# Optimization experiments

Measured on AMD Instinct MI355X. Metric: run time of the kernel, lower is better.

## Reference

```python
import jax, jax.numpy as jnp
import numpy as np

# Dimensions inferred from the module (few-shot reweighted YOLOv2 region loss)
B, C, NA, NCPA = 64, 20, 5, 1          # batch, base classes, anchors, classes-per-anchor
H, W = 19, 19                           # feature map (608 input / stride 32)
T = 50                                  # cfg.max_boxes
THRESH = 0.6
COORD_SCALE = 1.0
CLASS_SCALE = 1.0
NB = B * C                              # per-class 'image' rows, as in the torch code
A4 = NA * H * W
EPS = 1e-12
BCE_EPS = 1e-7
ANCHORS = [[1.3221, 1.73145], [3.19275, 4.00944], [5.05587, 8.09892], [9.47112, 4.84053], [11.2364, 10.0071]]


def iou_xywh(x1, y1, w1, h1, x2, y2, w2, h2):
    # center-size IoU, matches darknet bbox_iou(x1y1x2y2=False)
    l = jnp.maximum(x1 - w1 * 0.5, x2 - w2 * 0.5)
    r = jnp.minimum(x1 + w1 * 0.5, x2 + w2 * 0.5)
    t = jnp.maximum(y1 - h1 * 0.5, y2 - h2 * 0.5)
    b = jnp.minimum(y1 + h1 * 0.5, y2 + h2 * 0.5)
    inter = jnp.clip(r - l, 0.0) * jnp.clip(b - t, 0.0)
    union = w1 * h1 + w2 * h2 - inter
    return inter / jnp.maximum(union, EPS)


def setup_inputs() -> dict:
    key = jax.random.key(0)
    k1, k2, k3, k4 = jax.random.split(key, 4)
    output = jax.random.normal(k1, (NB, NA * (5 + NCPA), H, W), jnp.float32) * 0.5
    # target rows: [cls, x, y, w, h] * T, coords in (0,1); x kept > 0 so all boxes are 'valid'
    cls_ids = jax.random.randint(k2, (B, C, T), 0, C).astype(jnp.float32)
    xy = jax.random.uniform(k3, (B, C, T, 2), minval=0.05, maxval=0.95)
    wh = jax.random.uniform(k4, (B, C, T, 2), minval=0.05, maxval=0.5)
    target = jnp.concatenate([cls_ids[..., None], xy, wh], axis=-1).reshape(B, C, T * 5)
    anchors = jnp.asarray(ANCHORS, jnp.float32)
    return {"output": output, "target": target, "anchors": anchors}


def _forward(output, target, anchors):
    target = jax.lax.stop_gradient(target)
    anchors = jax.lax.stop_gradient(anchors)
    out5 = output.reshape(NB, NA, 5 + NCPA, H, W)
    x = jax.nn.sigmoid(out5[:, :, 0])
    y = jax.nn.sigmoid(out5[:, :, 1])
    w = out5[:, :, 2]
    h = out5[:, :, 3]
    conf = jax.nn.sigmoid(out5[:, :, 4])
    # class logits regrouped to original batch: (B*NA*H*W, C)
    cls = out5[:, :, 5:5 + NCPA].reshape(NB, NA, H, W)
    cls_logits = cls.reshape(B, C, NA * H * W).transpose(0, 2, 1).reshape(-1, C)
    # decode pred boxes (detached, mirroring torch's use of .data)
    grid_x = jnp.arange(W, dtype=jnp.float32)[None, None, None, :]
    grid_y = jnp.arange(H, dtype=jnp.float32)[None, None, :, None]
    aw = anchors[:, 0][None, :, None, None]
    ah = anchors[:, 1][None, :, None, None]
    px = jax.lax.stop_gradient(x) + grid_x
    py = jax.lax.stop_gradient(y) + grid_y
    pw = jnp.exp(jax.lax.stop_gradient(w)) * aw
    ph = jnp.exp(jax.lax.stop_gradient(h)) * ah
    # ground-truth boxes per row
    tgt = target.reshape(NB, T, 5)
    cls_t = tgt[:, :, 0]
    gx = tgt[:, :, 1] * W
    gy = tgt[:, :, 2] * H
    gw = tgt[:, :, 3] * W
    gh = tgt[:, :, 4] * H
    # 'break on first zero x' semantics
    valid = jnp.cumprod((tgt[:, :, 1] != 0).astype(jnp.int32), axis=1) > 0
    # stage 1: zero conf_mask where any gt IoU > thresh (scan over T to avoid (NB,T,A4) blowup)
    pxf = px.reshape(NB, A4); pyf = py.reshape(NB, A4)
    pwf = pw.reshape(NB, A4); phf = ph.reshape(NB, A4)

    def iou_step(ci, xs):
        gxt, gyt, gwt, ght, vt = xs
        iou = iou_xywh(pxf, pyf, pwf, phf, gxt[:, None], gyt[:, None], gwt[:, None], ght[:, None])
        return jnp.maximum(ci, jnp.where(vt[:, None], iou, 0.0)), None

    cur_ious, _ = jax.lax.scan(iou_step, jnp.zeros((NB, A4), jnp.float32), (gx.T, gy.T, gw.T, gh.T, valid.T))
    conf_mask0 = jnp.where(cur_ious.reshape(NB, NA, H, W) > THRESH, 0.0, 1.0)
    # best anchor per gt by wh-only IoU
    inter = jnp.minimum(gw[..., None], anchors[:, 0]) * jnp.minimum(gh[..., None], anchors[:, 1])
    union = gw[..., None] * gh[..., None] + anchors[:, 0] * anchors[:, 1] - inter
    best_n = jnp.argmax(inter / jnp.maximum(union, EPS), axis=-1).astype(jnp.int32)  # (NB,T)
    gi = gx.astype(jnp.int32)
    gj = gy.astype(jnp.int32)
    # stage 2: ordered scatter of targets (later boxes overwrite earlier, as in the torch loops)
    binds = jnp.arange(NB)
    z = jnp.zeros((NB, NA, H, W), jnp.float32)
    # seen < 12800 branch: tx=ty=0.5, tw=th=0, coord_mask=1
    carry0 = (jnp.ones_like(z), z, conf_mask0, jnp.full_like(z, 0.5), jnp.full_like(z, 0.5), z, z, z, z)

    def tgt_step(carry, xs):
        cm, clm, cfm, tx, ty, tw, th, tconf, tcls = carry
        gxt, gyt, gwt, ght, bn, git, gjt, vt, ct = xs
        idx = (binds, bn, gjt, git)

        def upd(arr, val):
            return arr.at[idx].set(jnp.where(vt, val, arr[idx]))

        aw_b = anchors[bn, 0]
        ah_b = anchors[bn, 1]
        iou = iou_xywh(gxt, gyt, gwt, ght, px[idx], py[idx], pw[idx], ph[idx])
        cm = upd(cm, 1.0)
        clm = upd(clm, 1.0)
        cfm = upd(cfm, 1.0)
        tx = upd(tx, gxt - git.astype(jnp.float32))
        ty = upd(ty, gyt - gjt.astype(jnp.float32))
        tw = upd(tw, jnp.log(jnp.maximum(gwt, EPS) / aw_b))
        th = upd(th, jnp.log(jnp.maximum(ght, EPS) / ah_b))
        tconf = upd(tconf, iou)
        tcls = upd(tcls, ct)
        return (cm, clm, cfm, tx, ty, tw, th, tconf, tcls), None

    xs = (gx.T, gy.T, gw.T, gh.T, best_n.T, gi.T, gj.T, valid.T, cls_t.T)
    (coord_mask, cls_mask, conf_mask, tx, ty, tw, th, tconf, tcls), _ = jax.lax.scan(tgt_step, carry0, xs)
    # regroup per-class rows back to original batch (neg_ratio='full' -> counts[i] == C)
    cm_grp = cls_mask.reshape(B, C, NA, H, W).sum(axis=1)
    tcls_grp = tcls.reshape(B, C, NA, H, W).sum(axis=1)
    sel = (cm_grp == 1.0).reshape(-1)           # exclude colliding cells
    labels = tcls_grp.reshape(-1).astype(jnp.int32)

    def bce_mean(p, t):
        p = jnp.clip(p, BCE_EPS, 1.0 - BCE_EPS)
        return jnp.mean(-(t * jnp.log(p) + (1.0 - t) * jnp.log(1.0 - p)))

    loss_x = COORD_SCALE * bce_mean(x * coord_mask, tx * coord_mask)
    loss_y = COORD_SCALE * bce_mean(y * coord_mask, ty * coord_mask)
    loss_w = COORD_SCALE * 0.5 * jnp.mean((w * coord_mask - tw * coord_mask) ** 2)
    loss_h = COORD_SCALE * 0.5 * jnp.mean((h * coord_mask - th * coord_mask) ** 2)
    loss_conf = 0.5 * jnp.mean((conf * conf_mask - tconf * conf_mask) ** 2)
    logp = jax.nn.log_softmax(cls_logits, axis=-1)
    nll = -jnp.take_along_axis(logp, labels[:, None], axis=1)[:, 0]
    nsel = jnp.maximum(jnp.sum(sel.astype(jnp.float32)), 1.0)
    loss_cls = CLASS_SCALE * jnp.sum(jnp.where(sel, nll, 0.0)) / nsel
    return loss_x + loss_y + loss_w + loss_h + loss_conf + loss_cls


def reference(output, target, anchors):
    return _forward(output, target, anchors)
```

## Files before the change

kernel.cpp:

```cpp
#include <hip/hip_runtime.h>
#include <math.h>

constexpr int cB   = 64;
constexpr int cC   = 20;
constexpr int cNA  = 5;
constexpr int cH   = 19;
constexpr int cW   = 19;
constexpr int cT   = 50;
constexpr int cNB  = cB * cC;
constexpr int cHW  = cH * cW;
constexpr int cA4  = cNA * cHW;
constexpr int cCH  = cNA * 6;
constexpr long cNTOT = (long)cNB * cA4;
constexpr int cCLS_ROWS = cB * cA4;

constexpr int ACC_BANKS = 64;
constexpr int TGT_N   = cNB * cT;
constexpr size_t SZT   = (size_t)TGT_N * 4;
constexpr size_t OFF_GX  = 4096;
constexpr size_t OFF_GY  = OFF_GX  + SZT;
constexpr size_t OFF_GW  = OFF_GY  + SZT;
constexpr size_t OFF_GH  = OFF_GW  + SZT;
constexpr size_t OFF_CLS = OFF_GH  + SZT;
constexpr size_t OFF_BL  = OFF_CLS + SZT;
constexpr size_t OFF_BR  = OFF_BL  + SZT;
constexpr size_t OFF_BT  = OFF_BR  + SZT;
constexpr size_t OFF_BB  = OFF_BT  + SZT;
constexpr size_t OFF_BGA = OFF_BB  + SZT;
constexpr size_t OFF_WIN = OFF_BGA + SZT;

__device__ __forceinline__ float fexp(float x) {
    return __builtin_amdgcn_exp2f(x * 1.4426950408889634f);
}
__device__ __forceinline__ float flog(float x) {
    return __builtin_amdgcn_logf(x) * 0.6931471805599453f;
}
__device__ __forceinline__ float frcp(float x) { return __builtin_amdgcn_rcpf(x); }
__device__ __forceinline__ float fsigmoid(float x) { return frcp(1.0f + fexp(-x)); }

__global__ void k_prep(const float* __restrict__ target, const float* __restrict__ anch,
                       float* __restrict__ gx_, float* __restrict__ gy_,
                       float* __restrict__ gw_, float* __restrict__ gh_,
                       float* __restrict__ cls_,
                       float* __restrict__ bl_, float* __restrict__ br_,
                       float* __restrict__ bt_, float* __restrict__ bb_,
                       float* __restrict__ bga_,
                       int* __restrict__ winner, double* __restrict__ acc) {
    const int nb = blockIdx.x;
    const int t  = threadIdx.x;
    if (nb == 0) {
        for (int k = t; k < 5 * ACC_BANKS; k += 64) acc[k] = 0.0;
    }
    float cv = 0.f, xr = 1.f, yr = 0.f, wr = 0.f, hr = 0.f;
    if (t < cT) {
        const float* tg = target + (size_t)nb * (cT * 5) + t * 5;
        cv = tg[0]; xr = tg[1]; yr = tg[2]; wr = tg[3]; hr = tg[4];
    }
    unsigned long long nz = __ballot(xr != 0.0f);
    if (t < cT) {
        unsigned long long below = (t == 63) ? ~0ull : ((2ull << t) - 1ull);
        bool valid = ((~nz) & below) == 0ull;
        float gx = xr * (float)cW, gy = yr * (float)cH;
        float gw = wr * (float)cW, gh = hr * (float)cH;
        int o = nb * cT + t;
        gx_[o] = gx; gy_[o] = gy; gw_[o] = gw; gh_[o] = gh;
        cls_[o] = cv;
        if (valid) {
            bl_[o] = gx - 0.5f * gw;  br_[o] = gx + 0.5f * gw;
            bt_[o] = gy - 0.5f * gh;  bb_[o] = gy + 0.5f * gh;
            bga_[o] = 0.6f * (gw * gh);
        } else {
            bl_[o] = 1e30f; br_[o] = -1e30f;
            bt_[o] = 1e30f; bb_[o] = -1e30f;
            bga_[o] = 0.0f;
        }
        float best = -1.0f; int bn = 0;
        for (int n = 0; n < cNA; ++n) {
            float aw = anch[2*n], ah = anch[2*n+1];
            float inter = fminf(gw, aw) * fminf(gh, ah);
            float uni   = gw*gh + aw*ah - inter;
            float r = inter / fmaxf(uni, 1e-12f);
            if (r > best) { best = r; bn = n; }
        }
        if (valid) {
            int gi = (int)gx, gj = (int)gy;
            atomicMax(&winner[(size_t)nb * cA4 + bn * cHW + gj * cW + gi], t);
        }
    }
}

__launch_bounds__(256)
__global__ void k_main(const float* __restrict__ outp, const float* __restrict__ anch,
                       const float* __restrict__ gx_, const float* __restrict__ gy_,
                       const float* __restrict__ gw_, const float* __restrict__ gh_,
                       const float* __restrict__ bl_, const float* __restrict__ br_,
                       const float* __restrict__ bt_, const float* __restrict__ bb_,
                       const float* __restrict__ bga_,
                       const int* __restrict__ winner, double* __restrict__ acc) {
    __shared__ double s_red[3][4];
    const int tid = threadIdx.x;
    const int nb  = blockIdx.x;
    const int tb  = nb * cT;
    const float* obase = outp + (size_t)nb * (cCH * cHW);

    float pl[8], pr[8], pt[8], pb[8], pa06[8], ov[8];

    #pragma unroll
    for (int u = 0; u < 8; ++u) {
        int cell = tid + (u << 8);
        int cc   = (cell < cA4) ? cell : (cA4 - 1);
        int na   = cc / cHW;
        int rem  = cc - na * cHW;
        int j    = rem / cW;
        int i    = rem - j * cW;
        const float* ob = obase + (size_t)(na * 6) * cHW + rem;
        float xl = ob[0], yl = ob[cHW], wl = ob[2*cHW], hl = ob[3*cHW];
        float aw = anch[2*na], ah = anch[2*na+1];
        float x  = fsigmoid(xl), y = fsigmoid(yl);
        float px = x + (float)i, py = y + (float)j;
        float pw = fexp(wl) * aw, ph = fexp(hl) * ah;
        pl[u] = px - 0.5f*pw; pr[u] = px + 0.5f*pw;
        pt[u] = py - 0.5f*ph; pb[u] = py + 0.5f*ph;
        pa06[u] = 0.6f * (pw * ph);
        ov[u] = -1e30f;
    }

    #pragma unroll 5
    for (int t = 0; t < cT; ++t) {
        float sl = bl_[tb + t], sr = br_[tb + t];
        float st = bt_[tb + t], sb = bb_[tb + t];
        float sg = bga_[tb + t];
        #pragma unroll
        for (int u = 0; u < 8; ++u) {
            float iw = fminf(pr[u], sr) - fmaxf(pl[u], sl);
            float ih = fminf(pb[u], sb) - fmaxf(pt[u], st);
            iw = fmaxf(iw, 0.0f); ih = fmaxf(ih, 0.0f);
            ov[u] = fmaxf(ov[u], __builtin_fmaf(1.6f, iw * ih, -sg));
        }
    }

    float bce = 0.0f, sq = 0.0f, sc = 0.0f;
    #pragma unroll
    for (int u = 0; u < 8; ++u) {
        int cell = tid + (u << 8);
        bool a_  = cell < cA4;
        int cc   = a_ ? cell : (cA4 - 1);
        int na   = cc / cHW;
        int rem  = cc - na * cHW;
        int j    = rem / cW;
        int i    = rem - j * cW;
        const float* ob = obase + (size_t)(na * 6) * cHW + rem;
        float xl = ob[0], yl = ob[cHW], wl = ob[2*cHW], hl = ob[3*cHW], cl = ob[4*cHW];
        float aw = anch[2*na], ah = anch[2*na+1];
        float x  = fsigmoid(xl), y = fsigmoid(yl), cf = fsigmoid(cl);
        float tx = 0.5f, ty = 0.5f, tw = 0.0f, th = 0.0f, tcf = 0.0f;
        int wt = winner[(size_t)nb * cA4 + cc];
        bool wfl = (wt >= 0) && a_;
        if (wfl) {
            float gx = gx_[tb+wt], gy = gy_[tb+wt], gw = gw_[tb+wt], gh = gh_[tb+wt];
            tx = gx - (float)i; ty = gy - (float)j;
            tw = flog(fmaxf(gw, 1e-12f) * frcp(aw));
            th = flog(fmaxf(gh, 1e-12f) * frcp(ah));
            float iw = fminf(pr[u], gx + 0.5f*gw) - fmaxf(pl[u], gx - 0.5f*gw);
            float ih = fminf(pb[u], gy + 0.5f*gh) - fmaxf(pt[u], gy - 0.5f*gh);
            iw = fmaxf(iw, 0.0f); ih = fmaxf(ih, 0.0f);
            float inter = iw * ih;
            float pa  = pa06[u] * (1.0f / 0.6f);
            float uni = gw*gh + pa - inter;
            tcf = inter * frcp(fmaxf(uni, 1e-12f));
        }
        if (a_) {
            float pc = fminf(fmaxf(x, 1e-7f), 1.0f - 1e-7f);
            bce += -(tx * flog(pc) + (1.0f - tx) * flog(1.0f - pc));
            pc = fminf(fmaxf(y, 1e-7f), 1.0f - 1e-7f);
            bce += -(ty * flog(pc) + (1.0f - ty) * flog(1.0f - pc));
            float dw = wl - tw, dh = hl - th;
            sq += dw*dw + dh*dh;
            float cm = wfl ? 1.0f : ((ov[u] > pa06[u]) ? 0.0f : 1.0f);
            float d  = (cf - tcf) * cm;
            sc += d * d;
        }
    }

    double v0 = (double)bce, v1 = (double)sq, v2 = (double)sc;
    for (int off = 32; off > 0; off >>= 1) {
        v0 += __shfl_down(v0, off);
        v1 += __shfl_down(v1, off);
        v2 += __shfl_down(v2, off);
    }
    int lane = tid & 63, wid = tid >> 6;
    if (lane == 0) { s_red[0][wid] = v0; s_red[1][wid] = v1; s_red[2][wid] = v2; }
    __syncthreads();
    if (tid == 0) {
        double a0 = s_red[0][0] + s_red[0][1] + s_red[0][2] + s_red[0][3];
        double a1 = s_red[1][0] + s_red[1][1] + s_red[1][2] + s_red[1][3];
        double a2 = s_red[2][0] + s_red[2][1] + s_red[2][2] + s_red[2][3];
        int bank = nb & (ACC_BANKS - 1);
        atomicAdd(&acc[0*ACC_BANKS + bank], a0);
        atomicAdd(&acc[1*ACC_BANKS + bank], a1);
        atomicAdd(&acc[2*ACC_BANKS + bank], a2);
    }
}

__launch_bounds__(256)
__global__ void k_cls(const float* __restrict__ outp, const float* __restrict__ cls_,
                      const int* __restrict__ winner, double* __restrict__ acc) {
    __shared__ double s_red[2][4];
    int tid = threadIdx.x;
    int row = blockIdx.x * 256 + tid;
    double nll = 0.0, ns = 0.0;
    if (row < cCLS_ROWS) {
        int b = row / cA4;
        int a = row - b * cA4;
        int cnt = 0, selc = -1, selw = -1;
        #pragma unroll
        for (int c = 0; c < cC; ++c) {
            int wv = winner[(size_t)(b * cC + c) * cA4 + a];
            if (wv >= 0) { cnt++; selc = c; selw = wv; }
        }
        if (cnt == 1) {
            int na  = a / cHW;
            int rem = a - na * cHW;
            const float* ob = outp + ((size_t)b * cC * cCH + na * 6 + 5) * cHW + rem;
            float l[cC]; float m = -1e30f;
            #pragma unroll
            for (int c = 0; c < cC; ++c) { l[c] = ob[(size_t)c * cCH * cHW]; m = fmaxf(m, l[c]); }
            float s = 0.0f;
            #pragma unroll
            for (int c = 0; c < cC; ++c) s += fexp(l[c] - m);
            int label = (int)cls_[(b * cC + selc) * cT + selw];
            nll = (double)(m + flog(s) - l[label]);
            ns  = 1.0;
        }
    }
    for (int off = 32; off > 0; off >>= 1) {
        nll += __shfl_down(nll, off);
        ns  += __shfl_down(ns, off);
    }
    int lane = tid & 63, wid = tid >> 6;
    if (lane == 0) { s_red[0][wid] = nll; s_red[1][wid] = ns; }
    __syncthreads();
    if (tid == 0) {
        double a0 = s_red[0][0] + s_red[0][1] + s_red[0][2] + s_red[0][3];
        double a1 = s_red[1][0] + s_red[1][1] + s_red[1][2] + s_red[1][3];
        int bank = blockIdx.x & (ACC_BANKS - 1);
        atomicAdd(&acc[3*ACC_BANKS + bank], a0);
        atomicAdd(&acc[4*ACC_BANKS + bank], a1);
    }
}

__global__ void k_final(const double* __restrict__ acc, float* __restrict__ o) {
    int lane = threadIdx.x;
    double s[5];
    #pragma unroll
    for (int j = 0; j < 5; ++j) {
        double v = acc[j * ACC_BANKS + lane];
        for (int off = 32; off > 0; off >>= 1) v += __shfl_down(v, off);
        s[j] = v;
    }
    if (lane == 0) {
        double Ninv = 1.0 / (double)cNTOT;
        double loss = s[0] * Ninv
                    + 0.5 * s[1] * Ninv
                    + 0.5 * s[2] * Ninv
                    + s[3] / fmax(s[4], 1.0);
        o[0] = (float)loss;
    }
}

extern "C" void kernel_launch(void* const* d_in, const int* in_sizes, int n_in,
                              void* d_out, int out_size, void* d_ws, size_t ws_size,
                              hipStream_t stream) {
    const float* output = (const float*)d_in[0];
    const float* target = (const float*)d_in[1];
    const float* anch   = (const float*)d_in[2];
    char* ws = (char*)d_ws;
    double* acc  = (double*)ws;
    float* gx_   = (float*)(ws + OFF_GX);
    float* gy_   = (float*)(ws + OFF_GY);
    float* gw_   = (float*)(ws + OFF_GW);
    float* gh_   = (float*)(ws + OFF_GH);
    float* cls_  = (float*)(ws + OFF_CLS);
    float* bl_   = (float*)(ws + OFF_BL);
    float* br_   = (float*)(ws + OFF_BR);
    float* bt_   = (float*)(ws + OFF_BT);
    float* bb_   = (float*)(ws + OFF_BB);
    float* bga_  = (float*)(ws + OFF_BGA);
    int*   winner= (int*)  (ws + OFF_WIN);

    hipMemsetAsync(winner, 0xFF, (size_t)cNTOT * 4, stream);

    k_prep<<<cNB, 64, 0, stream>>>(target, anch, gx_, gy_, gw_, gh_, cls_,
                                   bl_, br_, bt_, bb_, bga_, winner, acc);
    k_main<<<cNB, 256, 0, stream>>>(output, anch, gx_, gy_, gw_, gh_,
                                    bl_, br_, bt_, bb_, bga_, winner, acc);
    k_cls<<<(cCLS_ROWS + 255) / 256, 256, 0, stream>>>(output, cls_, winner, acc);
    k_final<<<1, 64, 0, stream>>>(acc, (float*)d_out);
}
```

Before: 145.9 us.

## Use packed fp16 IoU ignore test, split main blocks, fuse memset and final

```diff
diff --git a/kernel.cpp b/kernel.cpp
--- a/kernel.cpp
+++ b/kernel.cpp
@@ -13,21 +13,23 @@
 constexpr int cCH  = cNA * 6;
 constexpr long cNTOT = (long)cNB * cA4;
 constexpr int cCLS_ROWS = cB * cA4;
+constexpr int cCLS_BLOCKS = (cCLS_ROWS + 255) / 256;
 
 constexpr int ACC_BANKS = 64;
 constexpr int TGT_N   = cNB * cT;
 constexpr size_t SZT   = (size_t)TGT_N * 4;
+constexpr size_t OFF_CNT = 2560;
 constexpr size_t OFF_GX  = 4096;
 constexpr size_t OFF_GY  = OFF_GX  + SZT;
 constexpr size_t OFF_GW  = OFF_GY  + SZT;
 constexpr size_t OFF_GH  = OFF_GW  + SZT;
 constexpr size_t OFF_CLS = OFF_GH  + SZT;
-constexpr size_t OFF_BL  = OFF_CLS + SZT;
-constexpr size_t OFF_BR  = OFF_BL  + SZT;
-constexpr size_t OFF_BT  = OFF_BR  + SZT;
-constexpr size_t OFF_BB  = OFF_BT  + SZT;
-constexpr size_t OFF_BGA = OFF_BB  + SZT;
-constexpr size_t OFF_WIN = OFF_BGA + SZT;
+constexpr size_t OFF_HL  = OFF_CLS + SZT;
+constexpr size_t OFF_HR  = OFF_HL  + SZT;
+constexpr size_t OFF_HT  = OFF_HR  + SZT;
+constexpr size_t OFF_HB  = OFF_HT  + SZT;
+constexpr size_t OFF_HG  = OFF_HB  + SZT;
+constexpr size_t OFF_WIN = OFF_HG  + SZT;
 
 __device__ __forceinline__ float fexp(float x) {
     return __builtin_amdgcn_exp2f(x * 1.4426950408889634f);
@@ -37,20 +39,30 @@
 }
 __device__ __forceinline__ float frcp(float x) { return __builtin_amdgcn_rcpf(x); }
 __device__ __forceinline__ float fsigmoid(float x) { return frcp(1.0f + fexp(-x)); }
+
+typedef _Float16 h2 __attribute__((ext_vector_type(2)));
+union HU { unsigned u; h2 h; };
+__device__ __forceinline__ unsigned splat2(float v) {
+    HU x; _Float16 f = (_Float16)v; x.h[0] = f; x.h[1] = f; return x.u;
+}
 
 __global__ void k_prep(const float* __restrict__ target, const float* __restrict__ anch,
                        float* __restrict__ gx_, float* __restrict__ gy_,
                        float* __restrict__ gw_, float* __restrict__ gh_,
                        float* __restrict__ cls_,
-                       float* __restrict__ bl_, float* __restrict__ br_,
-                       float* __restrict__ bt_, float* __restrict__ bb_,
-                       float* __restrict__ bga_,
-                       int* __restrict__ winner, double* __restrict__ acc) {
+                       unsigned* __restrict__ hl_, unsigned* __restrict__ hr_,
+                       unsigned* __restrict__ ht_, unsigned* __restrict__ hb_,
+                       unsigned* __restrict__ hg_,
+                       int* __restrict__ winner, double* __restrict__ acc,
+                       int* __restrict__ cnt) {
     const int nb = blockIdx.x;
     const int t  = threadIdx.x;
     if (nb == 0) {
         for (int k = t; k < 5 * ACC_BANKS; k += 64) acc[k] = 0.0;
-    }
+        if (t == 0) *cnt = 0;
+    }
+    for (int k = t; k < cA4; k += 64) winner[(size_t)nb * cA4 + k] = -1;
+
     float cv = 0.f, xr = 1.f, yr = 0.f, wr = 0.f, hr = 0.f;
     if (t < cT) {
         const float* tg = target + (size_t)nb * (cT * 5) + t * 5;
@@ -66,13 +78,15 @@
         gx_[o] = gx; gy_[o] = gy; gw_[o] = gw; gh_[o] = gh;
         cls_[o] = cv;
         if (valid) {
-            bl_[o] = gx - 0.5f * gw;  br_[o] = gx + 0.5f * gw;
-            bt_[o] = gy - 0.5f * gh;  bb_[o] = gy + 0.5f * gh;
-            bga_[o] = 0.6f * (gw * gh);
+            hl_[o] = splat2(gx - 0.5f * gw);
+            hr_[o] = splat2(gx + 0.5f * gw);
+            ht_[o] = splat2(gy - 0.5f * gh);
+            hb_[o] = splat2(gy + 0.5f * gh);
+            hg_[o] = splat2(-0.6f * (gw * gh));
         } else {
-            bl_[o] = 1e30f; br_[o] = -1e30f;
-            bt_[o] = 1e30f; bb_[o] = -1e30f;
-            bga_[o] = 0.0f;
+            hl_[o] = splat2(1e30f);  hr_[o] = splat2(-1e30f);
+            ht_[o] = splat2(1e30f);  hb_[o] = splat2(-1e30f);
+            hg_[o] = splat2(0.0f);
         }
         float best = -1.0f; int bn = 0;
         for (int n = 0; n < cNA; ++n) {
@@ -87,62 +101,34 @@
             atomicMax(&winner[(size_t)nb * cA4 + bn * cHW + gj * cW + gi], t);
         }
     }
+    __syncthreads();
 }
 
 __launch_bounds__(256)
 __global__ void k_main(const float* __restrict__ outp, const float* __restrict__ anch,
                        const float* __restrict__ gx_, const float* __restrict__ gy_,
                        const float* __restrict__ gw_, const float* __restrict__ gh_,
-                       const float* __restrict__ bl_, const float* __restrict__ br_,
-                       const float* __restrict__ bt_, const float* __restrict__ bb_,
-                       const float* __restrict__ bga_,
+                       const unsigned* __restrict__ hl_, const unsigned* __restrict__ hr_,
+                       const unsigned* __restrict__ ht_, const unsigned* __restrict__ hb_,
+                       const unsigned* __restrict__ hg_,
                        const int* __restrict__ winner, double* __restrict__ acc) {
     __shared__ double s_red[3][4];
-    const int tid = threadIdx.x;
-    const int nb  = blockIdx.x;
-    const int tb  = nb * cT;
+    const int tid  = threadIdx.x;
+    const int nb   = blockIdx.x >> 1;
+    const int base = ((blockIdx.x & 1) << 10) + tid;
+    const int tb   = nb * cT;
     const float* obase = outp + (size_t)nb * (cCH * cHW);
 
-    float pl[8], pr[8], pt[8], pb[8], pa06[8], ov[8];
+    h2 pl2[2], pr2[2], pt2[2], pb2[2], ov2[2], pa06h[2];
+    float conf[4], tcf[4];
+    unsigned wbits = 0;
+    float bce = 0.0f, sq = 0.0f;
+    const h2 z2  = { (_Float16)0.0f, (_Float16)0.0f };
+    const h2 c16 = { (_Float16)1.6f, (_Float16)1.6f };
 
     #pragma unroll
-    for (int u = 0; u < 8; ++u) {
-        int cell = tid + (u << 8);
-        int cc   = (cell < cA4) ? cell : (cA4 - 1);
-        int na   = cc / cHW;
-        int rem  = cc - na * cHW;
-        int j    = rem / cW;
-        int i    = rem - j * cW;
-        const float* ob = obase + (size_t)(na * 6) * cHW + rem;
-        float xl = ob[0], yl = ob[cHW], wl = ob[2*cHW], hl = ob[3*cHW];
-        float aw = anch[2*na], ah = anch[2*na+1];
-        float x  = fsigmoid(xl), y = fsigmoid(yl);
-        float px = x + (float)i, py = y + (float)j;
-        float pw = fexp(wl) * aw, ph = fexp(hl) * ah;
-        pl[u] = px - 0.5f*pw; pr[u] = px + 0.5f*pw;
-        pt[u] = py - 0.5f*ph; pb[u] = py + 0.5f*ph;
-        pa06[u] = 0.6f * (pw * ph);
-        ov[u] = -1e30f;
-    }
-
-    #pragma unroll 5
-    for (int t = 0; t < cT; ++t) {
-        float sl = bl_[tb + t], sr = br_[tb + t];
-        float st = bt_[tb + t], sb = bb_[tb + t];
-        float sg = bga_[tb + t];
-        #pragma unroll
-        for (int u = 0; u < 8; ++u) {
-            float iw = fminf(pr[u], sr) - fmaxf(pl[u], sl);
-            float ih = fminf(pb[u], sb) - fmaxf(pt[u], st);
-            iw = fmaxf(iw, 0.0f); ih = fmaxf(ih, 0.0f);
-            ov[u] = fmaxf(ov[u], __builtin_fmaf(1.6f, iw * ih, -sg));
-        }
-    }
-
-    float bce = 0.0f, sq = 0.0f, sc = 0.0f;
-    #pragma unroll
-    for (int u = 0; u < 8; ++u) {
-        int cell = tid + (u << 8);
+    for (int u = 0; u < 4; ++u) {
+        int cell = base + (u << 8);
         bool a_  = cell < cA4;
         int cc   = a_ ? cell : (cA4 - 1);
         int na   = cc / cHW;
@@ -153,21 +139,33 @@
         float xl = ob[0], yl = ob[cHW], wl = ob[2*cHW], hl = ob[3*cHW], cl = ob[4*cHW];
         float aw = anch[2*na], ah = anch[2*na+1];
         float x  = fsigmoid(xl), y = fsigmoid(yl), cf = fsigmoid(cl);
-        float tx = 0.5f, ty = 0.5f, tw = 0.0f, th = 0.0f, tcf = 0.0f;
+        float px = x + (float)i, py = y + (float)j;
+        float pw = fexp(wl) * aw, ph = fexp(hl) * ah;
+        float l0 = px - 0.5f*pw, r0 = px + 0.5f*pw;
+        float t0 = py - 0.5f*ph, b0 = py + 0.5f*ph;
+        float pa = pw * ph;
+        int p = u >> 1, s = u & 1;
+        pl2[p][s] = (_Float16)l0;  pr2[p][s] = (_Float16)r0;
+        pt2[p][s] = (_Float16)t0;  pb2[p][s] = (_Float16)b0;
+        pa06h[p][s] = (_Float16)(0.6f * pa);
+        ov2[p][s] = (_Float16)0.0f;
+        conf[u] = cf; tcf[u] = 0.0f;
+
+        float tx = 0.5f, ty = 0.5f, tw = 0.0f, th = 0.0f;
         int wt = winner[(size_t)nb * cA4 + cc];
         bool wfl = (wt >= 0) && a_;
         if (wfl) {
+            wbits |= (1u << u);
             float gx = gx_[tb+wt], gy = gy_[tb+wt], gw = gw_[tb+wt], gh = gh_[tb+wt];
             tx = gx - (float)i; ty = gy - (float)j;
             tw = flog(fmaxf(gw, 1e-12f) * frcp(aw));
             th = flog(fmaxf(gh, 1e-12f) * frcp(ah));
-            float iw = fminf(pr[u], gx + 0.5f*gw) - fmaxf(pl[u], gx - 0.5f*gw);
-            float ih = fminf(pb[u], gy + 0.5f*gh) - fmaxf(pt[u], gy - 0.5f*gh);
+            float iw = fminf(r0, gx + 0.5f*gw) - fmaxf(l0, gx - 0.5f*gw);
+            float ih = fminf(b0, gy + 0.5f*gh) - fmaxf(t0, gy - 0.5f*gh);
             iw = fmaxf(iw, 0.0f); ih = fmaxf(ih, 0.0f);
             float inter = iw * ih;
-            float pa  = pa06[u] * (1.0f / 0.6f);
-            float uni = gw*gh + pa - inter;
-            tcf = inter * frcp(fmaxf(uni, 1e-12f));
+            float uni   = gw*gh + pa - inter;
+            tcf[u] = inter * frcp(fmaxf(uni, 1e-12f));
         }
         if (a_) {
             float pc = fminf(fmaxf(x, 1e-7f), 1.0f - 1e-7f);
@@ -176,10 +174,36 @@
             bce += -(ty * flog(pc) + (1.0f - ty) * flog(1.0f - pc));
             float dw = wl - tw, dh = hl - th;
             sq += dw*dw + dh*dh;
-            float cm = wfl ? 1.0f : ((ov[u] > pa06[u]) ? 0.0f : 1.0f);
-            float d  = (cf - tcf) * cm;
-            sc += d * d;
-        }
+        }
+    }
+
+    #pragma unroll 10
+    for (int t = 0; t < cT; ++t) {
+        HU a, b, c, d, e;
+        a.u = hl_[tb + t]; b.u = hr_[tb + t];
+        c.u = ht_[tb + t]; d.u = hb_[tb + t];
+        e.u = hg_[tb + t];
+        #pragma unroll
+        for (int p = 0; p < 2; ++p) {
+            h2 iw = __builtin_elementwise_min(pr2[p], b.h) - __builtin_elementwise_max(pl2[p], a.h);
+            h2 ih = __builtin_elementwise_min(pb2[p], d.h) - __builtin_elementwise_max(pt2[p], c.h);
+            iw = __builtin_elementwise_max(iw, z2);
+            ih = __builtin_elementwise_max(ih, z2);
+            ov2[p] = __builtin_elementwise_max(ov2[p], c16 * iw * ih + e.h);
+        }
+    }
+
+    float sc = 0.0f;
+    #pragma unroll
+    for (int u = 0; u < 4; ++u) {
+        int cell = base + (u << 8);
+        if (cell >= cA4) continue;
+        int p = u >> 1, s = u & 1;
+        bool wfl  = (wbits >> u) & 1;
+        bool over = ov2[p][s] > pa06h[p][s];
+        float cm  = wfl ? 1.0f : (over ? 0.0f : 1.0f);
+        float d   = (conf[u] - tcf[u]) * cm;
+        sc += d * d;
     }
 
     double v0 = (double)bce, v1 = (double)sq, v2 = (double)sc;
@@ -195,7 +219,7 @@
         double a0 = s_red[0][0] + s_red[0][1] + s_red[0][2] + s_red[0][3];
         double a1 = s_red[1][0] + s_red[1][1] + s_red[1][2] + s_red[1][3];
         double a2 = s_red[2][0] + s_red[2][1] + s_red[2][2] + s_red[2][3];
-        int bank = nb & (ACC_BANKS - 1);
+        int bank = blockIdx.x & (ACC_BANKS - 1);
         atomicAdd(&acc[0*ACC_BANKS + bank], a0);
         atomicAdd(&acc[1*ACC_BANKS + bank], a1);
         atomicAdd(&acc[2*ACC_BANKS + bank], a2);
@@ -204,21 +228,23 @@
 
 __launch_bounds__(256)
 __global__ void k_cls(const float* __restrict__ outp, const float* __restrict__ cls_,
-                      const int* __restrict__ winner, double* __restrict__ acc) {
+                      const int* __restrict__ winner, double* __restrict__ acc,
+                      int* __restrict__ cnt, float* __restrict__ out) {
     __shared__ double s_red[2][4];
+    __shared__ int s_last;
     int tid = threadIdx.x;
     int row = blockIdx.x * 256 + tid;
     double nll = 0.0, ns = 0.0;
     if (row < cCLS_ROWS) {
         int b = row / cA4;
         int a = row - b * cA4;
-        int cnt = 0, selc = -1, selw = -1;
+        int cnt1 = 0, selc = -1, selw = -1;
         #pragma unroll
         for (int c = 0; c < cC; ++c) {
             int wv = winner[(size_t)(b * cC + c) * cA4 + a];
-            if (wv >= 0) { cnt++; selc = c; selw = wv; }
-        }
-        if (cnt == 1) {
+            if (wv >= 0) { cnt1++; selc = c; selw = wv; }
+        }
+        if (cnt1 == 1) {
             int na  = a / cHW;
             int rem = a - na * cHW;
             const float* ob = outp + ((size_t)b * cC * cCH + na * 6 + 5) * cHW + rem;
@@ -246,25 +272,27 @@
         int bank = blockIdx.x & (ACC_BANKS - 1);
         atomicAdd(&acc[3*ACC_BANKS + bank], a0);
         atomicAdd(&acc[4*ACC_BANKS + bank], a1);
-    }
-}
-
-__global__ void k_final(const double* __restrict__ acc, float* __restrict__ o) {
-    int lane = threadIdx.x;
-    double s[5];
-    #pragma unroll
-    for (int j = 0; j < 5; ++j) {
-        double v = acc[j * ACC_BANKS + lane];
-        for (int off = 32; off > 0; off >>= 1) v += __shfl_down(v, off);
-        s[j] = v;
-    }
-    if (lane == 0) {
-        double Ninv = 1.0 / (double)cNTOT;
-        double loss = s[0] * Ninv
-                    + 0.5 * s[1] * Ninv
-                    + 0.5 * s[2] * Ninv
-                    + s[3] / fmax(s[4], 1.0);
-        o[0] = (float)loss;
+        __threadfence();
+        s_last = (atomicAdd(cnt, 1) == cCLS_BLOCKS - 1);
+    }
+    __syncthreads();
+    if (s_last && tid < 64) {
+        __threadfence();
+        double s[5];
+        #pragma unroll
+        for (int j = 0; j < 5; ++j) {
+            double v = atomicAdd(&acc[j * ACC_BANKS + tid], 0.0);
+            for (int off = 32; off > 0; off >>= 1) v += __shfl_down(v, off);
+            s[j] = v;
+        }
+        if (tid == 0) {
+            double Ninv = 1.0 / (double)cNTOT;
+            double loss = s[0] * Ninv
+                        + 0.5 * s[1] * Ninv
+                        + 0.5 * s[2] * Ninv
+                        + s[3] / fmax(s[4], 1.0);
+            out[0] = (float)loss;
+        }
     }
 }
 
@@ -275,25 +303,23 @@
     const float* target = (const float*)d_in[1];
     const float* anch   = (const float*)d_in[2];
     char* ws = (char*)d_ws;
-    double* acc  = (double*)ws;
-    float* gx_   = (float*)(ws + OFF_GX);
-    float* gy_   = (float*)(ws + OFF_GY);
-    float* gw_   = (float*)(ws + OFF_GW);
-    float* gh_   = (float*)(ws + OFF_GH);
-    float* cls_  = (float*)(ws + OFF_CLS);
-    float* bl_   = (float*)(ws + OFF_BL);
-    float* br_   = (float*)(ws + OFF_BR);
-    float* bt_   = (float*)(ws + OFF_BT);
-    float* bb_   = (float*)(ws + OFF_BB);
-    float* bga_  = (float*)(ws + OFF_BGA);
-    int*   winner= (int*)  (ws + OFF_WIN);
-
-    hipMemsetAsync(winner, 0xFF, (size_t)cNTOT * 4, stream);
+    double*   acc  = (double*)ws;
+    int*      cnt  = (int*)   (ws + OFF_CNT);
+    float*    gx_  = (float*) (ws + OFF_GX);
+    float*    gy_  = (float*) (ws + OFF_GY);
+    float*    gw_  = (float*) (ws + OFF_GW);
+    float*    gh_  = (float*) (ws + OFF_GH);
+    float*    cls_ = (float*) (ws + OFF_CLS);
+    unsigned* hl_  = (unsigned*)(ws + OFF_HL);
+    unsigned* hr_  = (unsigned*)(ws + OFF_HR);
+    unsigned* ht_  = (unsigned*)(ws + OFF_HT);
+    unsigned* hb_  = (unsigned*)(ws + OFF_HB);
+    unsigned* hg_  = (unsigned*)(ws + OFF_HG);
+    int*      win  = (int*)   (ws + OFF_WIN);
 
     k_prep<<<cNB, 64, 0, stream>>>(target, anch, gx_, gy_, gw_, gh_, cls_,
-                                   bl_, br_, bt_, bb_, bga_, winner, acc);
-    k_main<<<cNB, 256, 0, stream>>>(output, anch, gx_, gy_, gw_, gh_,
-                                    bl_, br_, bt_, bb_, bga_, winner, acc);
-    k_cls<<<(cCLS_ROWS + 255) / 256, 256, 0, stream>>>(output, cls_, winner, acc);
-    k_final<<<1, 64, 0, stream>>>(acc, (float*)d_out);
-}
+                                   hl_, hr_, ht_, hb_, hg_, win, acc, cnt);
+    k_main<<<cNB * 2, 256, 0, stream>>>(output, anch, gx_, gy_, gw_, gh_,
+                                        hl_, hr_, ht_, hb_, hg_, win, acc);
+    k_cls<<<cCLS_BLOCKS, 256, 0, stream>>>(output, cls_, win, acc, cnt, (float*)d_out);
+}
```

Result: faster. 141.3 us (-3.2%).
